# Kernel tuning notes

Measured on AMD Instinct MI355X. Metric: run time of the kernel, lower is better.

Reference implementation:

```python
import jax, jax.numpy as jnp
import numpy as np

N = 50000          # num_nodes
E = 1600000        # num directed edges
IN_C = 128         # in_channels
OUT_C = 128        # out_channels
HEADS = 8
HFD = OUT_C // HEADS  # head_feat_dim = 16
NEG_SLOPE = 0.2


def setup_inputs() -> dict:
    key = jax.random.key(0)
    k1, k2, k3, k4, k5 = jax.random.split(key, 5)
    node_feats = jax.random.normal(k1, (N, IN_C), dtype=jnp.float32)
    edge_index = jax.random.randint(k2, (2, E), 0, N, dtype=jnp.int64)
    # parameters (xavier-ish scale, kept small so exp() stays in range)
    W = jax.random.normal(k3, (OUT_C, IN_C), dtype=jnp.float32) * (1.0 / np.sqrt(IN_C))
    a_left = jax.random.normal(k4, (HFD, HEADS), dtype=jnp.float32) * 0.1
    a_right = jax.random.normal(k5, (HFD, HEADS), dtype=jnp.float32) * 0.1
    bias = jnp.zeros((OUT_C,), dtype=jnp.float32)
    return {"node_feats": node_feats, "edge_index": edge_index,
            "W": W, "a_left": a_left, "a_right": a_right, "bias": bias}


def reference(node_feats, edge_index, W, a_left, a_right, bias):
    n = node_feats.shape[0]
    # embedding: Linear without bias, then split into heads -> [n, h, c]
    emb = (node_feats @ W.T).reshape(n, HEADS, HFD)
    # per-node attention logit halves: sum_c emb[n,h,c] * a[c,h] -> [n, h]
    left = jnp.einsum('nhc,ch->nh', emb, a_left)
    right = jnp.einsum('nhc,ch->nh', emb, a_right)
    src = edge_index[0]
    dst = edge_index[1]
    # edge logit: score(src, dst) uses a_left on src, a_right on dst
    e = left[src] + right[dst]                       # [E, h]
    e = jnp.where(e >= 0, e, NEG_SLOPE * e)          # leaky relu(0.2)
    w = jnp.exp(e)                                   # [E, h] (module uses raw exp)
    denom = jax.ops.segment_sum(w, dst, num_segments=n)  # [n, h]
    attn = w / denom[dst]                            # [E, h]
    msg = emb[src] * attn[:, :, None]                # [E, h, c]
    out = jax.ops.segment_sum(msg, dst, num_segments=n)  # [n, h, c]
    # concat heads + bias
    out = out.reshape(n, HEADS * HFD) + bias
    return out
```

## Files before the change

kernel.cpp:

```cpp
#include <hip/hip_runtime.h>
#include <hip/hip_bf16.h>

#define N_NODES 50000
#define N_EDGES 1600000
#define HEADS 8
#define HFD 16
#define CH 128

#define PART 128
#define NB 391
#define BCAP 5120
#define PA_T 512
#define PA_CHUNK 3200
#define PA_PER 7
#define PA_BLOCKS 500
#define EMB_BLOCKS 391

#define QPART 32
#define QCAP 1536
#define AG_TASKS (NB * 4)
#define AG_BLOCKS 1568

#define NPH 4
#define PHSH 14
#define NBIN (NPH * QPART)

typedef __bf16 bf16x8 __attribute__((ext_vector_type(8)));
typedef __bf16 bf16x4 __attribute__((ext_vector_type(4)));
typedef float f32x4 __attribute__((ext_vector_type(4)));
typedef float f32x2 __attribute__((ext_vector_type(2)));

__device__ __forceinline__ float bf_lo(unsigned u) { return __uint_as_float(u << 16); }
__device__ __forceinline__ float bf_hi(unsigned u) { return __uint_as_float(u & 0xffff0000u); }

__global__ __launch_bounds__(256) void k_splitw(const float* __restrict__ W,
                                                const float* __restrict__ aL,
                                                const float* __restrict__ aR,
                                                __bf16* __restrict__ Whi,
                                                __bf16* __restrict__ Wlo,
                                                __bf16* __restrict__ Vhi,
                                                __bf16* __restrict__ Vlo,
                                                int* __restrict__ bucket_cnt) {
  int t = blockIdx.x * 256 + threadIdx.x;
  if (t < NB) bucket_cnt[t] = 0;
  if (t < CH * CH / 4) {
    f32x4 v = ((const f32x4*)W)[t];
    bf16x4 h, l;
#pragma unroll
    for (int i = 0; i < 4; ++i) {
      __bf16 hb = (__bf16)v[i];
      h[i] = hb;
      l[i] = (__bf16)(v[i] - (float)hb);
    }
    ((bf16x4*)Whi)[t] = h;
    ((bf16x4*)Wlo)[t] = l;
  }
  if (t < 16 * CH) {
    int j = t >> 7;
    int k = t & 127;
    int h = j & 7;
    const float* a = (j < 8) ? aL : aR;
    float v = 0.f;
#pragma unroll
    for (int c = 0; c < HFD; ++c) v += W[(h * HFD + c) * CH + k] * a[c * HEADS + h];
    __bf16 hb = (__bf16)v;
    Vhi[t] = hb;
    Vlo[t] = (__bf16)(v - (float)hb);
  }
}

__global__ __launch_bounds__(PA_T) void k_prep(const int* __restrict__ ei,
                                               int* __restrict__ bucket_cnt,
                                               unsigned* __restrict__ ebuf,
                                               const float* __restrict__ X,
                                               const __bf16* __restrict__ Whi,
                                               const __bf16* __restrict__ Wlo,
                                               const __bf16* __restrict__ Vhi,
                                               const __bf16* __restrict__ Vlo,
                                               __bf16* __restrict__ embb,
                                               float* __restrict__ leftp,
                                               float* __restrict__ rightp) {
  __shared__ unsigned sp[PA_CHUNK];
  __shared__ int hist[NB];
  __shared__ int lcur[NB];
  __shared__ int wbase[NB];
  __shared__ int wpart[8];
  int t = threadIdx.x;

  if (blockIdx.x >= PA_BLOCKS) {
    int ntile = (blockIdx.x - PA_BLOCKS) * 8 + (t >> 6);
    if (ntile >= N_NODES / 16) return;
    int lane = t & 63;
    int c = lane & 15, quad = lane >> 4;
    const float* xp = X + (size_t)(ntile * 16 + c) * CH + quad * 8;
    bf16x8 xh[4], xl[4];
#pragma unroll
    for (int ks = 0; ks < 4; ++ks) {
      float4 x0 = *(const float4*)(xp + ks * 32);
      float4 x1 = *(const float4*)(xp + ks * 32 + 4);
      float xv[8] = {x0.x, x0.y, x0.z, x0.w, x1.x, x1.y, x1.z, x1.w};
#pragma unroll
      for (int j = 0; j < 8; ++j) {
        __bf16 hb = (__bf16)xv[j];
        xh[ks][j] = hb;
        xl[ks][j] = (__bf16)(xv[j] - (float)hb);
      }
    }
#pragma unroll
    for (int h = 0; h < HEADS; ++h) {
      const __bf16* wp = Whi + (size_t)(h * 16 + c) * CH + quad * 8;
      const __bf16* wlp = Wlo + (size_t)(h * 16 + c) * CH + quad * 8;
      f32x4 acc = {0.f, 0.f, 0.f, 0.f};
#pragma unroll
      for (int ks = 0; ks < 4; ++ks) {
        bf16x8 wh = *(const bf16x8*)(wp + ks * 32);
        bf16x8 wl = *(const bf16x8*)(wlp + ks * 32);
        acc = __builtin_amdgcn_mfma_f32_16x16x32_bf16(xl[ks], wh, acc, 0, 0, 0);
        acc = __builtin_amdgcn_mfma_f32_16x16x32_bf16(xh[ks], wl, acc, 0, 0, 0);
        acc = __builtin_amdgcn_mfma_f32_16x16x32_bf16(xh[ks], wh, acc, 0, 0, 0);
      }
#pragma unroll
      for (int r = 0; r < 4; ++r) {
        int node = ntile * 16 + quad * 4 + r;
        embb[(size_t)node * CH + h * HFD + c] = (__bf16)acc[r];
      }
    }
    {
      const __bf16* vp = Vhi + (size_t)c * CH + quad * 8;
      const __bf16* vlp = Vlo + (size_t)c * CH + quad * 8;
      f32x4 acc = {0.f, 0.f, 0.f, 0.f};
#pragma unroll
      for (int ks = 0; ks < 4; ++ks) {
        bf16x8 vh = *(const bf16x8*)(vp + ks * 32);
        bf16x8 vl = *(const bf16x8*)(vlp + ks * 32);
        acc = __builtin_amdgcn_mfma_f32_16x16x32_bf16(xl[ks], vh, acc, 0, 0, 0);
        acc = __builtin_amdgcn_mfma_f32_16x16x32_bf16(xh[ks], vl, acc, 0, 0, 0);
        acc = __builtin_amdgcn_mfma_f32_16x16x32_bf16(xh[ks], vh, acc, 0, 0, 0);
      }
#pragma unroll
      for (int r = 0; r < 4; ++r) {
        int node = ntile * 16 + quad * 4 + r;
        if (c < 8) leftp[node * HEADS + c] = acc[r];
        else rightp[node * HEADS + (c - 8)] = acc[r];
      }
    }
    return;
  }

  int base = blockIdx.x * PA_CHUNK;
  for (int i = t; i < NB; i += PA_T) hist[i] = 0;
  __syncthreads();
  unsigned pk[PA_PER];
#pragma unroll
  for (int i = 0; i < PA_PER; ++i) {
    int e = t + i * PA_T;
    pk[i] = 0xffffffffu;
    if (e < PA_CHUNK) {
      int src = ei[base + e];
      int dst = ei[N_EDGES + base + e];
      pk[i] = ((unsigned)(dst >> 7) << 23) | ((unsigned)(dst & 127) << 16) |
              (unsigned)src;
      atomicAdd(&hist[dst >> 7], 1);
    }
  }
  __syncthreads();
  int hv = (t < NB) ? hist[t] : 0;
  int lane = t & 63, wid = t >> 6;
  int v = hv;
#pragma unroll
  for (int d = 1; d < 64; d <<= 1) {
    int o = __shfl_up(v, d);
    if (lane >= d) v += o;
  }
  if (lane == 63) wpart[wid] = v;
  __syncthreads();
  if (t < 8) {
    int pv = wpart[t];
#pragma unroll
    for (int d = 1; d < 8; d <<= 1) {
      int o = __shfl_up(pv, d);
      if (t >= d) pv += o;
    }
    wpart[t] = pv;
  }
  __syncthreads();
  int val = v + ((wid > 0) ? wpart[wid - 1] : 0);
  if (t < NB) {
    int lstart = val - hv;
    lcur[t] = lstart;
    int prior = hv ? atomicAdd(&bucket_cnt[t], hv) : 0;
    wbase[t] = t * BCAP + prior - lstart;
  }
  __syncthreads();
#pragma unroll
  for (int i = 0; i < PA_PER; ++i) {
    if (pk[i] != 0xffffffffu) {
      int b = pk[i] >> 23;
      int pos = atomicAdd(&lcur[b], 1);
      sp[pos] = pk[i];
    }
  }
  __syncthreads();
  for (int i = t; i < PA_CHUNK; i += PA_T) {
    unsigned p = sp[i];
    int b = p >> 23;
    int slot = wbase[b] + i;
    if (slot < (b + 1) * BCAP) ebuf[slot] = p;
  }
}

__global__ __launch_bounds__(256, 4) void k_aggr(const int* __restrict__ bucket_cnt,
                                                 const unsigned* __restrict__ ebuf,
                                                 const __bf16* __restrict__ embb,
                                                 const float* __restrict__ leftp,
                                                 const float* __restrict__ rightp,
                                                 const float* __restrict__ bias,
                                                 float* __restrict__ out) {
  __shared__ unsigned short su[QCAP];
  __shared__ int hist[NBIN];
  __shared__ int pfx[NBIN];
  __shared__ int cur[NBIN];
  __shared__ int wp2[2];
  int T = (blockIdx.x & 7) * (AG_BLOCKS / 8) + (blockIdx.x >> 3);
  if (T >= AG_TASKS) return;
  int b = T >> 2;
  int q = T & 3;
  int t = threadIdx.x;
  int cnt = bucket_cnt[b];
  if (cnt > BCAP) cnt = BCAP;
  int ebase = b * BCAP;
  for (int i = t; i < NBIN; i += 256) hist[i] = 0;
  __syncthreads();
  for (int e4 = t * 4; e4 < cnt; e4 += 1024) {
    uint4 pp = *(const uint4*)(ebuf + ebase + e4);
    unsigned pj[4] = {pp.x, pp.y, pp.z, pp.w};
#pragma unroll
    for (int j = 0; j < 4; ++j) {
      if (e4 + j < cnt) {
        int dl = (pj[j] >> 16) & 127;
        if ((dl >> 5) == q) {
          int ph = (int)(pj[j] & 0xffffu) >> PHSH;
          atomicAdd(&hist[ph * QPART + (dl & 31)], 1);
        }
      }
    }
  }
  __syncthreads();
  int hv = 0, vin = 0;
  if (t < NBIN) {
    hv = hist[t];
    int v = hv;
#pragma unroll
    for (int d = 1; d < 64; d <<= 1) {
      int o = __shfl_up(v, d);
      if ((t & 63) >= d) v += o;
    }
    if ((t & 63) == 63) wp2[t >> 6] = v;
    vin = v;
  }
  __syncthreads();
  if (t < NBIN) {
    int inc = vin + ((t >= 64) ? wp2[0] : 0);
    pfx[t] = inc - hv;
    cur[t] = inc - hv;
  }
  __syncthreads();
  for (int e4 = t * 4; e4 < cnt; e4 += 1024) {
    uint4 pp = *(const uint4*)(ebuf + ebase + e4);
    unsigned pj[4] = {pp.x, pp.y, pp.z, pp.w};
#pragma unroll
    for (int j = 0; j < 4; ++j) {
      if (e4 + j < cnt) {
        unsigned p = pj[j];
        int dl = (p >> 16) & 127;
        if ((dl >> 5) == q) {
          int ph = (int)(p & 0xffffu) >> PHSH;
          int pos = atomicAdd(&cur[ph * QPART + (dl & 31)], 1);
          if (pos < QCAP) su[pos] = (unsigned short)(p & 0xffffu);
        }
      }
    }
  }
  __syncthreads();

  int wv = t >> 6;
  int lane = t & 63;
  int g = lane >> 4;
  int m = lane & 15;
  int h = m >> 1;
  int dbase = b * PART + q * QPART + wv * 8;

  f32x2 acc[8][4];
  float dsum[8];
  float rr[8];
#pragma unroll
  for (int k = 0; k < 8; ++k) {
    int dst = dbase + k;
    rr[k] = (dst < N_NODES) ? rightp[dst * HEADS + h] : 0.f;
    dsum[k] = 0.f;
#pragma unroll
    for (int j = 0; j < 4; ++j) acc[k][j] = (f32x2){0.f, 0.f};
  }

#pragma unroll 1
  for (int p = 0; p < NPH; ++p) {
#pragma unroll
    for (int k = 0; k < 8; ++k) {
      int bin = p * QPART + wv * 8 + k;
      int beg = pfx[bin];
      int cd = hist[bin];
      if (beg + cd > QCAP) cd = QCAP - beg;
      for (int e0 = 0; e0 < cd; e0 += 4) {
        int i0 = e0 + g;
        bool a0 = i0 < cd;
        int s0 = su[beg + (a0 ? i0 : 0)];
        uint4 u0 = ((const uint4*)(embb + (size_t)s0 * CH))[m];
        float l0 = leftp[s0 * HEADS + h];
        float x0 = l0 + rr[k];
        x0 = (x0 >= 0.f) ? x0 : 0.2f * x0;
        float w0 = a0 ? __expf(x0) : 0.f;
        dsum[k] += w0;
        f32x2 wv0 = {w0, w0};
        acc[k][0] += wv0 * (f32x2){bf_lo(u0.x), bf_hi(u0.x)};
        acc[k][1] += wv0 * (f32x2){bf_lo(u0.y), bf_hi(u0.y)};
        acc[k][2] += wv0 * (f32x2){bf_lo(u0.z), bf_hi(u0.z)};
        acc[k][3] += wv0 * (f32x2){bf_lo(u0.w), bf_hi(u0.w)};
      }
    }
  }

#pragma unroll
  for (int k = 0; k < 8; ++k) {
    int dst = dbase + k;
    float ds = dsum[k];
    ds += __shfl_xor(ds, 16);
    ds += __shfl_xor(ds, 32);
    float a0 = acc[k][0].x, a1 = acc[k][0].y, a2 = acc[k][1].x, a3 = acc[k][1].y;
    float a4 = acc[k][2].x, a5 = acc[k][2].y, a6 = acc[k][3].x, a7 = acc[k][3].y;
#pragma unroll
    for (int mask = 16; mask <= 32; mask <<= 1) {
      a0 += __shfl_xor(a0, mask);
      a1 += __shfl_xor(a1, mask);
      a2 += __shfl_xor(a2, mask);
      a3 += __shfl_xor(a3, mask);
      a4 += __shfl_xor(a4, mask);
      a5 += __shfl_xor(a5, mask);
      a6 += __shfl_xor(a6, mask);
      a7 += __shfl_xor(a7, mask);
    }
    if (g == 0 && dst < N_NODES) {
      float inv = (ds > 0.f) ? 1.0f / ds : 0.f;
      float4 b0 = ((const float4*)bias)[2 * m];
      float4 b1 = ((const float4*)bias)[2 * m + 1];
      float4 o0 = {a0 * inv + b0.x, a1 * inv + b0.y,
                   a2 * inv + b0.z, a3 * inv + b0.w};
      float4 o1 = {a4 * inv + b1.x, a5 * inv + b1.y,
                   a6 * inv + b1.z, a7 * inv + b1.w};
      ((float4*)(out + (size_t)dst * CH))[2 * m] = o0;
      ((float4*)(out + (size_t)dst * CH))[2 * m + 1] = o1;
    }
  }
}

extern "C" void kernel_launch(void* const* d_in, const int* in_sizes, int n_in,
                              void* d_out, int out_size, void* d_ws, size_t ws_size,
                              hipStream_t stream) {
  const float* X = (const float*)d_in[0];
  const int* ei = (const int*)d_in[1];
  const float* W = (const float*)d_in[2];
  const float* al = (const float*)d_in[3];
  const float* ar = (const float*)d_in[4];
  const float* bias = (const float*)d_in[5];
  float* out = (float*)d_out;

  unsigned* ebuf = (unsigned*)d_ws;
  __bf16* embb = (__bf16*)(ebuf + (size_t)NB * BCAP);
  __bf16* Whi = embb + (size_t)N_NODES * CH;
  __bf16* Wlo = Whi + CH * CH;
  __bf16* Vhi = Wlo + CH * CH;
  __bf16* Vlo = Vhi + 16 * CH;
  float* leftp = (float*)(Vlo + 16 * CH);
  float* rightp = leftp + (size_t)N_NODES * HEADS;
  int* bucket_cnt = (int*)(rightp + (size_t)N_NODES * HEADS);

  k_splitw<<<16, 256, 0, stream>>>(W, al, ar, Whi, Wlo, Vhi, Vlo, bucket_cnt);
  k_prep<<<PA_BLOCKS + EMB_BLOCKS, PA_T, 0, stream>>>(ei, bucket_cnt, ebuf, X,
                                                      Whi, Wlo, Vhi, Vlo, embb,
                                                      leftp, rightp);
  k_aggr<<<AG_BLOCKS, 256, 0, stream>>>(bucket_cnt, ebuf, embb, leftp, rightp, bias, out);
}
```

Measured before the change: 231.6 us.

## Double aggregation block size and unroll edge loop by two

```diff
diff --git a/kernel.cpp b/kernel.cpp
--- a/kernel.cpp
+++ b/kernel.cpp
@@ -209,13 +209,13 @@
   }
 }
 
-__global__ __launch_bounds__(256, 4) void k_aggr(const int* __restrict__ bucket_cnt,
-                                                 const unsigned* __restrict__ ebuf,
-                                                 const __bf16* __restrict__ embb,
-                                                 const float* __restrict__ leftp,
-                                                 const float* __restrict__ rightp,
-                                                 const float* __restrict__ bias,
-                                                 float* __restrict__ out) {
+__global__ __launch_bounds__(512) void k_aggr(const int* __restrict__ bucket_cnt,
+                                              const unsigned* __restrict__ ebuf,
+                                              const __bf16* __restrict__ embb,
+                                              const float* __restrict__ leftp,
+                                              const float* __restrict__ rightp,
+                                              const float* __restrict__ bias,
+                                              float* __restrict__ out) {
   __shared__ unsigned short su[QCAP];
   __shared__ int hist[NBIN];
   __shared__ int pfx[NBIN];
@@ -229,9 +229,9 @@
   int cnt = bucket_cnt[b];
   if (cnt > BCAP) cnt = BCAP;
   int ebase = b * BCAP;
-  for (int i = t; i < NBIN; i += 256) hist[i] = 0;
-  __syncthreads();
-  for (int e4 = t * 4; e4 < cnt; e4 += 1024) {
+  if (t < NBIN) hist[t] = 0;
+  __syncthreads();
+  for (int e4 = t * 4; e4 < cnt; e4 += 2048) {
     uint4 pp = *(const uint4*)(ebuf + ebase + e4);
     unsigned pj[4] = {pp.x, pp.y, pp.z, pp.w};
 #pragma unroll
@@ -265,7 +265,7 @@
     cur[t] = inc - hv;
   }
   __syncthreads();
-  for (int e4 = t * 4; e4 < cnt; e4 += 1024) {
+  for (int e4 = t * 4; e4 < cnt; e4 += 2048) {
     uint4 pp = *(const uint4*)(ebuf + ebase + e4);
     unsigned pj[4] = {pp.x, pp.y, pp.z, pp.w};
 #pragma unroll
@@ -288,13 +288,13 @@
   int g = lane >> 4;
   int m = lane & 15;
   int h = m >> 1;
-  int dbase = b * PART + q * QPART + wv * 8;
-
-  f32x2 acc[8][4];
-  float dsum[8];
-  float rr[8];
-#pragma unroll
-  for (int k = 0; k < 8; ++k) {
+  int dbase = b * PART + q * QPART + wv * 4;
+
+  f32x2 acc[4][4];
+  float dsum[4];
+  float rr[4];
+#pragma unroll
+  for (int k = 0; k < 4; ++k) {
     int dst = dbase + k;
     rr[k] = (dst < N_NODES) ? rightp[dst * HEADS + h] : 0.f;
     dsum[k] = 0.f;
@@ -305,32 +305,42 @@
 #pragma unroll 1
   for (int p = 0; p < NPH; ++p) {
 #pragma unroll
-    for (int k = 0; k < 8; ++k) {
-      int bin = p * QPART + wv * 8 + k;
+    for (int k = 0; k < 4; ++k) {
+      int bin = p * QPART + wv * 4 + k;
       int beg = pfx[bin];
       int cd = hist[bin];
       if (beg + cd > QCAP) cd = QCAP - beg;
-      for (int e0 = 0; e0 < cd; e0 += 4) {
-        int i0 = e0 + g;
-        bool a0 = i0 < cd;
+      for (int e0 = 0; e0 < cd; e0 += 8) {
+        int i0 = e0 + g, i1 = e0 + 4 + g;
+        bool a0 = i0 < cd, a1 = i1 < cd;
         int s0 = su[beg + (a0 ? i0 : 0)];
+        int s1 = su[beg + (a1 ? i1 : 0)];
         uint4 u0 = ((const uint4*)(embb + (size_t)s0 * CH))[m];
+        uint4 u1 = ((const uint4*)(embb + (size_t)s1 * CH))[m];
         float l0 = leftp[s0 * HEADS + h];
+        float l1 = leftp[s1 * HEADS + h];
         float x0 = l0 + rr[k];
         x0 = (x0 >= 0.f) ? x0 : 0.2f * x0;
         float w0 = a0 ? __expf(x0) : 0.f;
-        dsum[k] += w0;
-        f32x2 wv0 = {w0, w0};
-        acc[k][0] += wv0 * (f32x2){bf_lo(u0.x), bf_hi(u0.x)};
-        acc[k][1] += wv0 * (f32x2){bf_lo(u0.y), bf_hi(u0.y)};
-        acc[k][2] += wv0 * (f32x2){bf_lo(u0.z), bf_hi(u0.z)};
-        acc[k][3] += wv0 * (f32x2){bf_lo(u0.w), bf_hi(u0.w)};
-      }
-    }
-  }
-
-#pragma unroll
-  for (int k = 0; k < 8; ++k) {
+        float x1 = l1 + rr[k];
+        x1 = (x1 >= 0.f) ? x1 : 0.2f * x1;
+        float w1 = a1 ? __expf(x1) : 0.f;
+        dsum[k] += w0 + w1;
+        f32x2 wv0 = {w0, w0}, wv1 = {w1, w1};
+        acc[k][0] += wv0 * (f32x2){bf_lo(u0.x), bf_hi(u0.x)}
+                   + wv1 * (f32x2){bf_lo(u1.x), bf_hi(u1.x)};
+        acc[k][1] += wv0 * (f32x2){bf_lo(u0.y), bf_hi(u0.y)}
+                   + wv1 * (f32x2){bf_lo(u1.y), bf_hi(u1.y)};
+        acc[k][2] += wv0 * (f32x2){bf_lo(u0.z), bf_hi(u0.z)}
+                   + wv1 * (f32x2){bf_lo(u1.z), bf_hi(u1.z)};
+        acc[k][3] += wv0 * (f32x2){bf_lo(u0.w), bf_hi(u0.w)}
+                   + wv1 * (f32x2){bf_lo(u1.w), bf_hi(u1.w)};
+      }
+    }
+  }
+
+#pragma unroll
+  for (int k = 0; k < 4; ++k) {
     int dst = dbase + k;
     float ds = dsum[k];
     ds += __shfl_xor(ds, 16);
@@ -387,5 +397,5 @@
   k_prep<<<PA_BLOCKS + EMB_BLOCKS, PA_T, 0, stream>>>(ei, bucket_cnt, ebuf, X,
                                                       Whi, Wlo, Vhi, Vlo, embb,
                                                       leftp, rightp);
-  k_aggr<<<AG_BLOCKS, 256, 0, stream>>>(bucket_cnt, ebuf, embb, leftp, rightp, bias, out);
+  k_aggr<<<AG_BLOCKS, 512, 0, stream>>>(bucket_cnt, ebuf, embb, leftp, rightp, bias, out);
 }
```

Result: faster. 205.6 us (-11.2%).
